# Kernel optimization log

Measured on AMD Instinct MI355X. Metric: run time of the kernel, lower is better.

Reference implementation:

```python
import jax, jax.numpy as jnp
import numpy as np

V, E, H, B, T, C = 50000, 100, 128, 128, 1024, 2


def setup_inputs() -> dict:
    key = jax.random.key(0)
    ks = jax.random.split(key, 32)
    rn = lambda k, shape: jax.random.normal(k, shape, jnp.float32) * 0.05
    inp = {}
    inp["x"] = jax.random.randint(ks[0], (B, T), 0, V)
    inp["emb"] = rn(ks[1], (V, E))
    i = 2
    for l, d_in in enumerate([E, 2 * H]):
        for sfx in ["", "_rev"]:
            inp[f"w_ih_l{l}{sfx}"] = rn(ks[i], (4 * H, d_in)); i += 1
            inp[f"w_hh_l{l}{sfx}"] = rn(ks[i], (4 * H, H)); i += 1
            inp[f"b_ih_l{l}{sfx}"] = rn(ks[i], (4 * H,)); i += 1
            inp[f"b_hh_l{l}{sfx}"] = rn(ks[i], (4 * H,)); i += 1
    inp["fc_w"] = rn(ks[i], (C, 2 * H))
    inp["fc_b"] = rn(ks[i + 1], (C,))
    return inp


def _lstm_dir(x, w_ih, w_hh, b_ih, b_hh, reverse):
    # x: [B, T, D]; PyTorch gate order: i, f, g, o
    Bn = x.shape[0]
    Hn = w_hh.shape[1]
    xp = jnp.einsum('btd,gd->btg', x, w_ih) + b_ih + b_hh  # [B, T, 4H], input proj hoisted out of scan
    xp = jnp.swapaxes(xp, 0, 1)  # [T, B, 4H]

    def step(carry, xt):
        h, c = carry
        g = xt + h @ w_hh.T
        i, f, gg, o = jnp.split(g, 4, axis=-1)
        c = jax.nn.sigmoid(f) * c + jax.nn.sigmoid(i) * jnp.tanh(gg)
        h = jax.nn.sigmoid(o) * jnp.tanh(c)
        return (h, c), h

    init = (jnp.zeros((Bn, Hn), x.dtype), jnp.zeros((Bn, Hn), x.dtype))
    (hT, cT), hs = jax.lax.scan(step, init, xp, reverse=reverse)
    return jnp.swapaxes(hs, 0, 1), hT  # [B, T, H], final hidden [B, H]


def reference(x, emb,
              w_ih_l0, w_hh_l0, b_ih_l0, b_hh_l0,
              w_ih_l0_rev, w_hh_l0_rev, b_ih_l0_rev, b_hh_l0_rev,
              w_ih_l1, w_hh_l1, b_ih_l1, b_hh_l1,
              w_ih_l1_rev, w_hh_l1_rev, b_ih_l1_rev, b_hh_l1_rev,
              fc_w, fc_b):
    h = emb[x]  # [B, T, E]
    # layer 0 (dropout between layers is identity in eval mode)
    f0, _ = _lstm_dir(h, w_ih_l0, w_hh_l0, b_ih_l0, b_hh_l0, False)
    b0, _ = _lstm_dir(h, w_ih_l0_rev, w_hh_l0_rev, b_ih_l0_rev, b_hh_l0_rev, True)
    h = jnp.concatenate([f0, b0], axis=-1)  # [B, T, 2H]
    # layer 1; final hidden states match torch hidden[-2] (fwd) and hidden[-1] (bwd)
    _, hf = _lstm_dir(h, w_ih_l1, w_hh_l1, b_ih_l1, b_hh_l1, False)
    _, hb = _lstm_dir(h, w_ih_l1_rev, w_hh_l1_rev, b_ih_l1_rev, b_hh_l1_rev, True)
    combined = jnp.concatenate([hf, hb], axis=-1)  # [B, 2H]
    return combined @ fc_w.T + fc_b  # [B, C]
```

## Files before the change

kernel.cpp:

```cpp
#include <hip/hip_runtime.h>
#include <hip/hip_bf16.h>
#include <stdint.h>


typedef unsigned short u16;
typedef short bf16x8 __attribute__((ext_vector_type(8)));
typedef unsigned short ushort8v __attribute__((ext_vector_type(8)));
typedef float f32x4 __attribute__((ext_vector_type(4)));
typedef float f32x2 __attribute__((ext_vector_type(2)));

#define NB 128
#define NT 1024
#define NH 128
#define TC 128
#define NCHUNK (NT / TC)
#define SMEM_BYTES 54656

#define L2E  1.44269504088896f
#define L2E2 2.88539008177793f

__device__ __forceinline__ u16 f2bf(float f) {
  union { float f; unsigned int i; } v; v.f = f;
  unsigned int i = v.i;
  return (u16)((i + 0x7FFFu + ((i >> 16) & 1u)) >> 16);
}

#if __has_builtin(__builtin_amdgcn_exp2f)
__device__ __forceinline__ float fast_exp2(float x) { return __builtin_amdgcn_exp2f(x); }
#else
__device__ __forceinline__ float fast_exp2(float x) { return exp2f(x); }
#endif
#if __has_builtin(__builtin_amdgcn_rcpf)
__device__ __forceinline__ float fast_rcp(float x) { return __builtin_amdgcn_rcpf(x); }
#else
__device__ __forceinline__ float fast_rcp(float x) { return 1.0f / x; }
#endif

__device__ __forceinline__ void sync_lds() {
  __builtin_amdgcn_s_waitcnt(0xc07f);
  __builtin_amdgcn_s_barrier();
}

__global__ void padw_kernel(const float* __restrict__ w0, const float* __restrict__ w1,
                            u16* __restrict__ out) {
  int idx = blockIdx.x * 256 + threadIdx.x;
  int d = idx >> 16;
  int n = (idx >> 7) & 511;
  int k = idx & 127;
  float sc = ((n >> 7) == 2) ? L2E2 : L2E;
  const float* w = d ? w1 : w0;
  out[idx] = (k < 100) ? f2bf(w[n * 100 + k] * sc) : (u16)0;
}

__global__ void cvt6_kernel(const float* s0, const float* s1, const float* s2,
                            const float* s3, const float* s4, const float* s5,
                            u16* d0, u16* d1, u16* d2, u16* d3, u16* d4, u16* d5,
                            int n0, int n1, int n2, int n3, int n4, int n5) {
  int y = blockIdx.y;
  const float* s; u16* d; int n; int gs;
  switch (y) {
    case 0: s = s0; d = d0; n = n0; gs = 14; break;
    case 1: s = s1; d = d1; n = n1; gs = 14; break;
    case 2: s = s2; d = d2; n = n2; gs = 14; break;
    case 3: s = s3; d = d3; n = n3; gs = 14; break;
    case 4: s = s4; d = d4; n = n4; gs = 15; break;
    default: s = s5; d = d5; n = n5; gs = 15; break;
  }
  int i = blockIdx.x * 256 + threadIdx.x;
  if (i < n) {
    float sc = (((i >> gs) & 3) == 2) ? L2E2 : L2E;
    d[i] = f2bf(s[i] * sc);
  }
}

template <int PK, int LL>
__global__ __launch_bounds__(512, 2) void fused_chunk(
    int do_lstm, int lc, int pc,
    const float* __restrict__ Aemb, const u16* __restrict__ Ah,
    const int* __restrict__ X,
    const u16* __restrict__ W0, const u16* __restrict__ W1,
    const float* __restrict__ bih0, const float* __restrict__ bhh0,
    const float* __restrict__ bih1, const float* __restrict__ bhh1,
    u16* __restrict__ xpc0, u16* __restrict__ xpc1,
    const u16* __restrict__ WHH0, const u16* __restrict__ WHH1,
    u16* __restrict__ OUT, float* __restrict__ FINALS,
    u16* __restrict__ HS, float* __restrict__ CS)
{
  extern __shared__ __align__(16) unsigned char smem[];

  const int tid = threadIdx.x;
  const int lane = tid & 63, wv = tid >> 6;
  const int l15 = lane & 15, q = lane >> 4;

  if (blockIdx.x >= 32) {
    constexpr int BK = 64;
    constexpr int LDA = 72;
    constexpr bool GATHER = (PK == 128);
    u16* As = (u16*)smem;
    u16* Bs = As + 128 * LDA;
    int* toks = (int*)(Bs + 128 * LDA);

    const int pb = blockIdx.x - 32;
    const int b = pb & 127;
    const int gate = (pb >> 7) & 3;
    const int nt0 = gate * 128;
    const int dir = pb >> 9;
    const u16* W = dir ? W1 : W0;
    u16* XPC = (pc & 1) ? xpc1 : xpc0;

    const int wr = wv >> 2, wc = wv & 3;

    if (GATHER) {
      if (tid < 128) {
        int t = dir ? (NT - 1 - pc * TC - tid) : (pc * TC + tid);
        toks[tid] = X[b * NT + t];
      }
    }

    f32x4 acc[4][2];
#pragma unroll
    for (int a = 0; a < 4; a++)
#pragma unroll
      for (int bb = 0; bb < 2; bb++)
        acc[a][bb] = (f32x4){0.f, 0.f, 0.f, 0.f};

    const int srow = tid >> 3;
    const int sseg = (tid & 7) * 8;

    for (int k0 = 0; k0 < PK; k0 += BK) {
      __syncthreads();
#pragma unroll
      for (int p = 0; p < 2; p++) {
        int row = srow + p * 64;
        if (GATHER) {
          int tok = toks[row];
          const float* er = Aemb + (size_t)tok * 100;
          int kb = k0 + sseg;
          union { ushort8v v; u16 e[8]; } tu;
          if (kb + 8 <= 100) {
            f32x4 a0 = *(const f32x4*)&er[kb];
            f32x4 a1 = *(const f32x4*)&er[kb + 4];
#pragma unroll
            for (int j = 0; j < 4; j++) { tu.e[j] = f2bf(a0[j]); tu.e[4 + j] = f2bf(a1[j]); }
          } else {
#pragma unroll
            for (int j = 0; j < 8; j++) tu.e[j] = (kb + j < 100) ? f2bf(er[kb + j]) : (u16)0;
          }
          *(ushort8v*)&As[row * LDA + sseg] = tu.v;
        } else {
          int t = dir ? (NT - 1 - pc * TC - row) : (pc * TC + row);
          const u16* srcA = Ah + (size_t)(b * NT + t) * PK + k0 + sseg;
          *(ushort8v*)&As[row * LDA + sseg] = *(const ushort8v*)srcA;
        }
        const u16* srcB = W + (size_t)(nt0 + row) * PK + k0 + sseg;
        *(ushort8v*)&Bs[row * LDA + sseg] = *(const ushort8v*)srcB;
      }
      __syncthreads();
#pragma unroll
      for (int kk = 0; kk < BK; kk += 32) {
        bf16x8 af[4], bfr[2];
#pragma unroll
        for (int mt = 0; mt < 4; mt++)
          af[mt] = *(const bf16x8*)&As[(wr * 64 + mt * 16 + l15) * LDA + kk + q * 8];
#pragma unroll
        for (int nt = 0; nt < 2; nt++)
          bfr[nt] = *(const bf16x8*)&Bs[(wc * 32 + nt * 16 + l15) * LDA + kk + q * 8];
#pragma unroll
        for (int mt = 0; mt < 4; mt++)
#pragma unroll
          for (int nt = 0; nt < 2; nt++)
            acc[mt][nt] = __builtin_amdgcn_mfma_f32_16x16x32_bf16(af[mt], bfr[nt], acc[mt][nt], 0, 0, 0);
      }
    }

    const float* bih = dir ? bih1 : bih0;
    const float* bhh = dir ? bhh1 : bhh0;
    const float gsc = (gate == 2) ? L2E2 : L2E;
    const int rb = b & 7;
    u16* xo = XPC + (size_t)(dir * 16 + (b >> 3)) * TC * 4096
                  + ((rb >> 1) & 1) * 64 + ((rb >> 2) & 1) * 32 + (rb & 1) + l15 * 2;
#pragma unroll
    for (int nt = 0; nt < 2; nt++) {
      int col = wc * 32 + nt * 16 + l15;
      int n = nt0 + col;
      float bias = (bih[n] + bhh[n]) * gsc;
      int bnt = ((wc * 2 + nt) * 4 + gate) * 128;
#pragma unroll
      for (int mt = 0; mt < 4; mt++) {
        int slb = wr * 64 + mt * 16 + q * 4;
#pragma unroll
        for (int r = 0; r < 4; r++)
          xo[(size_t)(slb + r) * 4096 + bnt] = f2bf(acc[mt][nt][r] + bias);
      }
    }
    return;
  }

  if (!do_lstm) return;

  __builtin_amdgcn_s_setprio(3);

  const int wg = blockIdx.x & 15, dir = blockIdx.x >> 4;
  const int hc = 16 * wv + l15;
  const u16* XPC = (lc & 1) ? xpc1 : xpc0;

  const int row0 = ((lane >> 4) & 1) * 4 + (lane >> 5) * 2;

  const u16* Wp = dir ? WHH1 : WHH0;
  bf16x8 wf[4][4];
#pragma unroll
  for (int gi = 0; gi < 4; gi++)
#pragma unroll
    for (int kt = 0; kt < 4; kt++)
      wf[gi][kt] = *(const bf16x8*)&Wp[(gi * 128 + hc) * 128 + kt * 32 + q * 8];

  u16* hb = (u16*)smem;

  const int g0 = (dir * 128 + wg * 8 + row0) * 128 + hc;
  f32x2 cst2;
  if (lc == 0) {
    for (int i = tid; i < 2 * 8 * 136; i += 512) hb[i] = 0;
    cst2 = (f32x2){0.f, 0.f};
  } else {
    hb[row0 * 136 + hc] = HS[g0];
    hb[(row0 + 1) * 136 + hc] = HS[g0 + 128];
    cst2[0] = CS[g0];
    cst2[1] = CS[g0 + 128];
  }

  const u16* xb = XPC + (size_t)(dir * 16 + wg) * TC * 4096 + wv * 512 + lane * 2;

#define LDXP(dst, s) do {                                        \
    const u16* nb_ = xb + (size_t)(s) * 4096;                    \
    _Pragma("unroll")                                            \
    for (int gi_ = 0; gi_ < 4; gi_++)                            \
      (dst)[gi_] = *(const unsigned int*)(nb_ + gi_ * 128);      \
  } while (0)

  unsigned int xp[4][4];
  LDXP(xp[0], 0);
  LDXP(xp[1], 1);
  LDXP(xp[2], 2);

  const int t0 = dir ? (NT - 1 - lc * TC) : (lc * TC);
  const int tstep = dir ? -256 : 256;
  u16* optr[2];
  if (LL == 0) {
#pragma unroll
    for (int rr = 0; rr < 2; rr++)
      optr[rr] = OUT + ((size_t)(wg * 8 + row0 + rr) * NT + t0) * 256 + dir * 128 + hc;
  }

  const f32x4 zero4 = {0.f, 0.f, 0.f, 0.f};
  const bool hi32 = (lane >= 32);
  const int arow = (l15 & 7) * 136;

  __syncthreads();

  int p = 0;
#pragma unroll 1
  for (int sl = 0; sl < TC; sl += 4) {
#pragma unroll
    for (int jj = 0; jj < 4; jj++) {
      const int scur = sl + jj;

      const unsigned int* xcur = xp[jj];
      f32x2 xv[4];
#pragma unroll
      for (int gi = 0; gi < 4; gi++) {
        union { unsigned int u; float f; } lo, hi;
        lo.u = xcur[gi] << 16;
        hi.u = xcur[gi] & 0xFFFF0000u;
        xv[gi][0] = lo.f; xv[gi][1] = hi.f;
      }
      {
        int sn = scur + 3; if (sn > TC - 1) sn = TC - 1;
        LDXP(xp[(jj + 3) & 3], sn);
      }

      bf16x8 ah[4];
#pragma unroll
      for (int kt = 0; kt < 4; kt++)
        ah[kt] = *(const bf16x8*)&hb[p * 1088 + arow + kt * 32 + q * 8];

      f32x4 acc[4];
#pragma unroll
      for (int gi = 0; gi < 4; gi++) {
        acc[gi] = __builtin_amdgcn_mfma_f32_16x16x32_bf16(ah[0], wf[gi][0], zero4, 0, 0, 0);
#pragma unroll
        for (int kt = 1; kt < 4; kt++)
          acc[gi] = __builtin_amdgcn_mfma_f32_16x16x32_bf16(ah[kt], wf[gi][kt], acc[gi], 0, 0, 0);
      }

      f32x2 ar[4];
#pragma unroll
      for (int gi = 0; gi < 4; gi++) {
        ar[gi][0] = hi32 ? acc[gi][2] : acc[gi][0];
        ar[gi][1] = hi32 ? acc[gi][3] : acc[gi][1];
      }

      f32x2 pi = ar[0] + xv[0];
      f32x2 pf = ar[1] + xv[1];
      f32x2 pg = ar[2] + xv[2];
      f32x2 po = ar[3] + xv[3];
      f32x2 ei, ef, eg, eo;
      ei[0] = fast_exp2(pi[0]); ei[1] = fast_exp2(pi[1]);
      ef[0] = fast_exp2(pf[0]); ef[1] = fast_exp2(pf[1]);
      eg[0] = fast_exp2(pg[0]); eg[1] = fast_exp2(pg[1]);
      eo[0] = fast_exp2(po[0]); eo[1] = fast_exp2(po[1]);
      f32x2 A  = 1.f + ef;
      f32x2 Bv = 1.f + ei;
      f32x2 Cg = 1.f + eg;
      f32x2 BC = Bv * Cg;
      f32x2 num = cst2 * ef * BC + ei * (eg - 1.f) * A;
      f32x2 den = A * BC;
      f32x2 rden; rden[0] = fast_rcp(den[0]); rden[1] = fast_rcp(den[1]);
      f32x2 cn = num * rden;
      cst2 = cn;
      f32x2 tc2 = L2E2 * cn;
      f32x2 ec; ec[0] = fast_exp2(tc2[0]); ec[1] = fast_exp2(tc2[1]);
      f32x2 d2 = (1.f + eo) * (1.f + ec);
      f32x2 r2; r2[0] = fast_rcp(d2[0]); r2[1] = fast_rcp(d2[1]);
      f32x2 hv2 = eo * (ec - 1.f) * r2;

      u16 hbv0 = f2bf(hv2[0]);
      u16 hbv1 = f2bf(hv2[1]);
      u16* hn = hb + (p ^ 1) * 1088;
      hn[row0 * 136 + hc] = hbv0;
      hn[(row0 + 1) * 136 + hc] = hbv1;
      if (LL == 0) {
        *optr[0] = hbv0; optr[0] += tstep;
        *optr[1] = hbv1; optr[1] += tstep;
      }
      if (scur == TC - 1) {
        HS[g0] = hbv0;
        HS[g0 + 128] = hbv1;
        CS[g0] = cst2[0];
        CS[g0 + 128] = cst2[1];
        if (LL == 1 && lc == NCHUNK - 1) {
          FINALS[(wg * 8 + row0) * 256 + dir * 128 + hc] = hv2[0];
          FINALS[(wg * 8 + row0 + 1) * 256 + dir * 128 + hc] = hv2[1];
        }
      }
      sync_lds();
      p ^= 1;
    }
  }
#undef LDXP
}

__global__ void fc_kernel(const float* __restrict__ finals, const float* __restrict__ fcw,
                          const float* __restrict__ fcb, float* __restrict__ out) {
  int tid = threadIdx.x;
  int b = tid >> 1, cc = tid & 1;
  float s = fcb[cc];
  for (int k = 0; k < 256; k++) s += finals[b * 256 + k] * fcw[cc * 256 + k];
  out[b * 2 + cc] = s;
}

extern "C" void kernel_launch(void* const* d_in, const int* in_sizes, int n_in,
                              void* d_out, int out_size, void* d_ws, size_t ws_size,
                              hipStream_t stream) {
  const int*   x        = (const int*)d_in[0];
  const float* emb      = (const float*)d_in[1];
  const float* w_ih_l0  = (const float*)d_in[2];
  const float* w_hh_l0  = (const float*)d_in[3];
  const float* b_ih_l0  = (const float*)d_in[4];
  const float* b_hh_l0  = (const float*)d_in[5];
  const float* w_ih_l0r = (const float*)d_in[6];
  const float* w_hh_l0r = (const float*)d_in[7];
  const float* b_ih_l0r = (const float*)d_in[8];
  const float* b_hh_l0r = (const float*)d_in[9];
  const float* w_ih_l1  = (const float*)d_in[10];
  const float* w_hh_l1  = (const float*)d_in[11];
  const float* b_ih_l1  = (const float*)d_in[12];
  const float* b_hh_l1  = (const float*)d_in[13];
  const float* w_ih_l1r = (const float*)d_in[14];
  const float* w_hh_l1r = (const float*)d_in[15];
  const float* b_ih_l1r = (const float*)d_in[16];
  const float* b_hh_l1r = (const float*)d_in[17];
  const float* fc_w     = (const float*)d_in[18];
  const float* fc_b     = (const float*)d_in[19];
  float* out = (float*)d_out;

  char* ws = (char*)d_ws;
  size_t off = 0;
  u16*   h1cat = (u16*)(ws + off);   off += 67108864;
  u16*   xpc0  = (u16*)(ws + off);   off += 33554432;
  u16*   xpc1  = (u16*)(ws + off);   off += 33554432;
  u16*   w0pad = (u16*)(ws + off);   off += 262144;
  u16*   wih1b = (u16*)(ws + off);   off += 524288;
  u16*   whhb  = (u16*)(ws + off);   off += 524288;
  u16*   hs    = (u16*)(ws + off);   off += 65536;
  float* cs    = (float*)(ws + off); off += 131072;
  float* fin   = (float*)(ws + off); off += 131072;
  if (ws_size < off) return;

  hipLaunchKernelGGL(padw_kernel, dim3(512), dim3(256), 0, stream,
                     w_ih_l0, w_ih_l0r, w0pad);
  hipLaunchKernelGGL(cvt6_kernel, dim3(512, 6), dim3(256), 0, stream,
                     w_hh_l0, w_hh_l0r, w_hh_l1, w_hh_l1r, w_ih_l1, w_ih_l1r,
                     whhb, whhb + 65536, whhb + 131072, whhb + 196608,
                     wih1b, wih1b + 131072,
                     65536, 65536, 65536, 65536, 131072, 131072);

  for (int k = 0; k <= NCHUNK; k++) {
    int do_proj = (k < NCHUNK);
    int do_lstm = (k > 0);
    hipLaunchKernelGGL((fused_chunk<128, 0>), dim3(do_proj ? 1056 : 32), dim3(512),
                       SMEM_BYTES, stream,
                       do_lstm, k - 1, k,
                       emb, (const u16*)nullptr, x, w0pad, w0pad + 65536,
                       b_ih_l0, b_hh_l0, b_ih_l0r, b_hh_l0r,
                       xpc0, xpc1, whhb, whhb + 65536,
                       h1cat, fin, hs, cs);
  }
  for (int k = 0; k <= NCHUNK; k++) {
    int do_proj = (k < NCHUNK);
    int do_lstm = (k > 0);
    hipLaunchKernelGGL((fused_chunk<256, 1>), dim3(do_proj ? 1056 : 32), dim3(512),
                       SMEM_BYTES, stream,
                       do_lstm, k - 1, k,
                       (const float*)nullptr, h1cat, (const int*)nullptr,
                       wih1b, wih1b + 131072,
                       b_ih_l1, b_hh_l1, b_ih_l1r, b_hh_l1r,
                       xpc0, xpc1, whhb + 131072, whhb + 196608,
                       h1cat, fin, hs, cs);
  }
  hipLaunchKernelGGL(fc_kernel, dim3(1), dim3(256), 0, stream, fin, fc_w, fc_b, out);
}
```

Baseline: 1.418 ms.

## Run both LSTM directions in one block per batch group, interleaved

The recurrent part now uses 16 workgroups instead of 32. Each workgroup processes both the forward and reverse directions for its 8 batch rows, holding both W_hh sets in registers and interleaving the two independent recurrences within each timestep. The intent is to fill the latency of the serial MFMA-then-activation dependency chain with independent work from the other direction, and to share one LDS barrier across both. In exchange it doubles register use for weights and per-step work per block, reduces the prefetch depth of the xp buffer from 3 steps to 2, and halves the number of CUs doing the recurrence.

```diff
diff --git a/kernel.cpp b/kernel.cpp
--- a/kernel.cpp
+++ b/kernel.cpp
@@ -92,7 +92,7 @@
   const int lane = tid & 63, wv = tid >> 6;
   const int l15 = lane & 15, q = lane >> 4;
 
-  if (blockIdx.x >= 32) {
+  if (blockIdx.x >= 16) {
     constexpr int BK = 64;
     constexpr int LDA = 72;
     constexpr bool GATHER = (PK == 128);
@@ -100,7 +100,7 @@
     u16* Bs = As + 128 * LDA;
     int* toks = (int*)(Bs + 128 * LDA);
 
-    const int pb = blockIdx.x - 32;
+    const int pb = blockIdx.x - 16;
     const int b = pb & 127;
     const int gate = (pb >> 7) & 3;
     const int nt0 = gate * 128;
@@ -200,55 +200,72 @@
 
   __builtin_amdgcn_s_setprio(3);
 
-  const int wg = blockIdx.x & 15, dir = blockIdx.x >> 4;
+  const int wg = blockIdx.x;
   const int hc = 16 * wv + l15;
   const u16* XPC = (lc & 1) ? xpc1 : xpc0;
 
   const int row0 = ((lane >> 4) & 1) * 4 + (lane >> 5) * 2;
 
-  const u16* Wp = dir ? WHH1 : WHH0;
-  bf16x8 wf[4][4];
-#pragma unroll
-  for (int gi = 0; gi < 4; gi++)
-#pragma unroll
-    for (int kt = 0; kt < 4; kt++)
-      wf[gi][kt] = *(const bf16x8*)&Wp[(gi * 128 + hc) * 128 + kt * 32 + q * 8];
+  bf16x8 wf[2][4][4];
+#pragma unroll
+  for (int d = 0; d < 2; d++) {
+    const u16* Wp = d ? WHH1 : WHH0;
+#pragma unroll
+    for (int gi = 0; gi < 4; gi++)
+#pragma unroll
+      for (int kt = 0; kt < 4; kt++)
+        wf[d][gi][kt] = *(const bf16x8*)&Wp[(gi * 128 + hc) * 128 + kt * 32 + q * 8];
+  }
 
   u16* hb = (u16*)smem;
 
-  const int g0 = (dir * 128 + wg * 8 + row0) * 128 + hc;
-  f32x2 cst2;
+  int g0[2];
+  f32x2 cst[2];
   if (lc == 0) {
-    for (int i = tid; i < 2 * 8 * 136; i += 512) hb[i] = 0;
-    cst2 = (f32x2){0.f, 0.f};
+    for (int i = tid; i < 2 * 2 * 1088; i += 512) hb[i] = 0;
+#pragma unroll
+    for (int d = 0; d < 2; d++) {
+      g0[d] = (d * 128 + wg * 8 + row0) * 128 + hc;
+      cst[d] = (f32x2){0.f, 0.f};
+    }
   } else {
-    hb[row0 * 136 + hc] = HS[g0];
-    hb[(row0 + 1) * 136 + hc] = HS[g0 + 128];
-    cst2[0] = CS[g0];
-    cst2[1] = CS[g0 + 128];
-  }
-
-  const u16* xb = XPC + (size_t)(dir * 16 + wg) * TC * 4096 + wv * 512 + lane * 2;
-
-#define LDXP(dst, s) do {                                        \
-    const u16* nb_ = xb + (size_t)(s) * 4096;                    \
-    _Pragma("unroll")                                            \
-    for (int gi_ = 0; gi_ < 4; gi_++)                            \
-      (dst)[gi_] = *(const unsigned int*)(nb_ + gi_ * 128);      \
+#pragma unroll
+    for (int d = 0; d < 2; d++) {
+      g0[d] = (d * 128 + wg * 8 + row0) * 128 + hc;
+      hb[d * 2176 + row0 * 136 + hc] = HS[g0[d]];
+      hb[d * 2176 + (row0 + 1) * 136 + hc] = HS[g0[d] + 128];
+      cst[d][0] = CS[g0[d]];
+      cst[d][1] = CS[g0[d] + 128];
+    }
+  }
+
+  const u16* xb[2];
+  xb[0] = XPC + (size_t)(wg) * TC * 4096 + wv * 512 + lane * 2;
+  xb[1] = XPC + (size_t)(16 + wg) * TC * 4096 + wv * 512 + lane * 2;
+
+#define LDXP(dst, s) do {                                            \
+    _Pragma("unroll")                                                \
+    for (int d_ = 0; d_ < 2; d_++) {                                 \
+      const u16* nb_ = xb[d_] + (size_t)(s) * 4096;                  \
+      _Pragma("unroll")                                              \
+      for (int gi_ = 0; gi_ < 4; gi_++)                              \
+        (dst)[d_][gi_] = *(const unsigned int*)(nb_ + gi_ * 128);    \
+    }                                                                \
   } while (0)
 
-  unsigned int xp[4][4];
+  unsigned int xp[2][2][4];
   LDXP(xp[0], 0);
   LDXP(xp[1], 1);
-  LDXP(xp[2], 2);
-
-  const int t0 = dir ? (NT - 1 - lc * TC) : (lc * TC);
-  const int tstep = dir ? -256 : 256;
-  u16* optr[2];
+
+  u16* optr[2][2];
   if (LL == 0) {
 #pragma unroll
-    for (int rr = 0; rr < 2; rr++)
-      optr[rr] = OUT + ((size_t)(wg * 8 + row0 + rr) * NT + t0) * 256 + dir * 128 + hc;
+    for (int d = 0; d < 2; d++) {
+      const int t0d = d ? (NT - 1 - lc * TC) : (lc * TC);
+#pragma unroll
+      for (int rr = 0; rr < 2; rr++)
+        optr[d][rr] = OUT + ((size_t)(wg * 8 + row0 + rr) * NT + t0d) * 256 + d * 128 + hc;
+    }
   }
 
   const f32x4 zero4 = {0.f, 0.f, 0.f, 0.f};
@@ -259,87 +276,97 @@
 
   int p = 0;
 #pragma unroll 1
-  for (int sl = 0; sl < TC; sl += 4) {
-#pragma unroll
-    for (int jj = 0; jj < 4; jj++) {
+  for (int sl = 0; sl < TC; sl += 2) {
+#pragma unroll
+    for (int jj = 0; jj < 2; jj++) {
       const int scur = sl + jj;
 
-      const unsigned int* xcur = xp[jj];
-      f32x2 xv[4];
-#pragma unroll
-      for (int gi = 0; gi < 4; gi++) {
-        union { unsigned int u; float f; } lo, hi;
-        lo.u = xcur[gi] << 16;
-        hi.u = xcur[gi] & 0xFFFF0000u;
-        xv[gi][0] = lo.f; xv[gi][1] = hi.f;
-      }
+      f32x2 xv[2][4];
+#pragma unroll
+      for (int d = 0; d < 2; d++)
+#pragma unroll
+        for (int gi = 0; gi < 4; gi++) {
+          union { unsigned int u; float f; } lo, hi;
+          lo.u = xp[jj][d][gi] << 16;
+          hi.u = xp[jj][d][gi] & 0xFFFF0000u;
+          xv[d][gi][0] = lo.f; xv[d][gi][1] = hi.f;
+        }
       {
-        int sn = scur + 3; if (sn > TC - 1) sn = TC - 1;
-        LDXP(xp[(jj + 3) & 3], sn);
-      }
-
-      bf16x8 ah[4];
-#pragma unroll
-      for (int kt = 0; kt < 4; kt++)
-        ah[kt] = *(const bf16x8*)&hb[p * 1088 + arow + kt * 32 + q * 8];
-
-      f32x4 acc[4];
-#pragma unroll
-      for (int gi = 0; gi < 4; gi++) {
-        acc[gi] = __builtin_amdgcn_mfma_f32_16x16x32_bf16(ah[0], wf[gi][0], zero4, 0, 0, 0);
-#pragma unroll
-        for (int kt = 1; kt < 4; kt++)
-          acc[gi] = __builtin_amdgcn_mfma_f32_16x16x32_bf16(ah[kt], wf[gi][kt], acc[gi], 0, 0, 0);
-      }
-
-      f32x2 ar[4];
-#pragma unroll
-      for (int gi = 0; gi < 4; gi++) {
-        ar[gi][0] = hi32 ? acc[gi][2] : acc[gi][0];
-        ar[gi][1] = hi32 ? acc[gi][3] : acc[gi][1];
-      }
-
-      f32x2 pi = ar[0] + xv[0];
-      f32x2 pf = ar[1] + xv[1];
-      f32x2 pg = ar[2] + xv[2];
-      f32x2 po = ar[3] + xv[3];
-      f32x2 ei, ef, eg, eo;
-      ei[0] = fast_exp2(pi[0]); ei[1] = fast_exp2(pi[1]);
-      ef[0] = fast_exp2(pf[0]); ef[1] = fast_exp2(pf[1]);
-      eg[0] = fast_exp2(pg[0]); eg[1] = fast_exp2(pg[1]);
-      eo[0] = fast_exp2(po[0]); eo[1] = fast_exp2(po[1]);
-      f32x2 A  = 1.f + ef;
-      f32x2 Bv = 1.f + ei;
-      f32x2 Cg = 1.f + eg;
-      f32x2 BC = Bv * Cg;
-      f32x2 num = cst2 * ef * BC + ei * (eg - 1.f) * A;
-      f32x2 den = A * BC;
-      f32x2 rden; rden[0] = fast_rcp(den[0]); rden[1] = fast_rcp(den[1]);
-      f32x2 cn = num * rden;
-      cst2 = cn;
-      f32x2 tc2 = L2E2 * cn;
-      f32x2 ec; ec[0] = fast_exp2(tc2[0]); ec[1] = fast_exp2(tc2[1]);
-      f32x2 d2 = (1.f + eo) * (1.f + ec);
-      f32x2 r2; r2[0] = fast_rcp(d2[0]); r2[1] = fast_rcp(d2[1]);
-      f32x2 hv2 = eo * (ec - 1.f) * r2;
-
-      u16 hbv0 = f2bf(hv2[0]);
-      u16 hbv1 = f2bf(hv2[1]);
-      u16* hn = hb + (p ^ 1) * 1088;
-      hn[row0 * 136 + hc] = hbv0;
-      hn[(row0 + 1) * 136 + hc] = hbv1;
-      if (LL == 0) {
-        *optr[0] = hbv0; optr[0] += tstep;
-        *optr[1] = hbv1; optr[1] += tstep;
-      }
-      if (scur == TC - 1) {
-        HS[g0] = hbv0;
-        HS[g0 + 128] = hbv1;
-        CS[g0] = cst2[0];
-        CS[g0 + 128] = cst2[1];
-        if (LL == 1 && lc == NCHUNK - 1) {
-          FINALS[(wg * 8 + row0) * 256 + dir * 128 + hc] = hv2[0];
-          FINALS[(wg * 8 + row0 + 1) * 256 + dir * 128 + hc] = hv2[1];
+        int sn = scur + 2; if (sn > TC - 1) sn = TC - 1;
+        LDXP(xp[jj], sn);
+      }
+
+      f32x2 hv2s[2];
+#pragma unroll
+      for (int d = 0; d < 2; d++) {
+        bf16x8 ah[4];
+#pragma unroll
+        for (int kt = 0; kt < 4; kt++)
+          ah[kt] = *(const bf16x8*)&hb[d * 2176 + p * 1088 + arow + kt * 32 + q * 8];
+
+        f32x4 acc[4];
+#pragma unroll
+        for (int gi = 0; gi < 4; gi++) {
+          acc[gi] = __builtin_amdgcn_mfma_f32_16x16x32_bf16(ah[0], wf[d][gi][0], zero4, 0, 0, 0);
+#pragma unroll
+          for (int kt = 1; kt < 4; kt++)
+            acc[gi] = __builtin_amdgcn_mfma_f32_16x16x32_bf16(ah[kt], wf[d][gi][kt], acc[gi], 0, 0, 0);
+        }
+
+        f32x2 ar[4];
+#pragma unroll
+        for (int gi = 0; gi < 4; gi++) {
+          ar[gi][0] = hi32 ? acc[gi][2] : acc[gi][0];
+          ar[gi][1] = hi32 ? acc[gi][3] : acc[gi][1];
+        }
+
+        f32x2 pi = ar[0] + xv[d][0];
+        f32x2 pf = ar[1] + xv[d][1];
+        f32x2 pg = ar[2] + xv[d][2];
+        f32x2 po = ar[3] + xv[d][3];
+        f32x2 ei, ef, eg, eo;
+        ei[0] = fast_exp2(pi[0]); ei[1] = fast_exp2(pi[1]);
+        ef[0] = fast_exp2(pf[0]); ef[1] = fast_exp2(pf[1]);
+        eg[0] = fast_exp2(pg[0]); eg[1] = fast_exp2(pg[1]);
+        eo[0] = fast_exp2(po[0]); eo[1] = fast_exp2(po[1]);
+        f32x2 A  = 1.f + ef;
+        f32x2 Bv = 1.f + ei;
+        f32x2 Cg = 1.f + eg;
+        f32x2 BC = Bv * Cg;
+        f32x2 num = cst[d] * ef * BC + ei * (eg - 1.f) * A;
+        f32x2 den = A * BC;
+        f32x2 rden; rden[0] = fast_rcp(den[0]); rden[1] = fast_rcp(den[1]);
+        f32x2 cn = num * rden;
+        cst[d] = cn;
+        f32x2 tc2 = L2E2 * cn;
+        f32x2 ec; ec[0] = fast_exp2(tc2[0]); ec[1] = fast_exp2(tc2[1]);
+        f32x2 d2 = (1.f + eo) * (1.f + ec);
+        f32x2 r2; r2[0] = fast_rcp(d2[0]); r2[1] = fast_rcp(d2[1]);
+        hv2s[d] = eo * (ec - 1.f) * r2;
+      }
+
+#pragma unroll
+      for (int d = 0; d < 2; d++) {
+        u16 hbv0 = f2bf(hv2s[d][0]);
+        u16 hbv1 = f2bf(hv2s[d][1]);
+        u16* hn = hb + d * 2176 + (p ^ 1) * 1088;
+        hn[row0 * 136 + hc] = hbv0;
+        hn[(row0 + 1) * 136 + hc] = hbv1;
+        if (LL == 0) {
+          *optr[d][0] = hbv0;
+          *optr[d][1] = hbv1;
+          optr[d][0] += (d ? -256 : 256);
+          optr[d][1] += (d ? -256 : 256);
+        }
+        if (scur == TC - 1) {
+          HS[g0[d]] = hbv0;
+          HS[g0[d] + 128] = hbv1;
+          CS[g0[d]] = cst[d][0];
+          CS[g0[d] + 128] = cst[d][1];
+          if (LL == 1 && lc == NCHUNK - 1) {
+            FINALS[(wg * 8 + row0) * 256 + d * 128 + hc] = hv2s[d][0];
+            FINALS[(wg * 8 + row0 + 1) * 256 + d * 128 + hc] = hv2s[d][1];
+          }
         }
       }
       sync_lds();
@@ -407,7 +434,7 @@
   for (int k = 0; k <= NCHUNK; k++) {
     int do_proj = (k < NCHUNK);
     int do_lstm = (k > 0);
-    hipLaunchKernelGGL((fused_chunk<128, 0>), dim3(do_proj ? 1056 : 32), dim3(512),
+    hipLaunchKernelGGL((fused_chunk<128, 0>), dim3(do_proj ? 1040 : 16), dim3(512),
                        SMEM_BYTES, stream,
                        do_lstm, k - 1, k,
                        emb, (const u16*)nullptr, x, w0pad, w0pad + 65536,
@@ -418,7 +445,7 @@
   for (int k = 0; k <= NCHUNK; k++) {
     int do_proj = (k < NCHUNK);
     int do_lstm = (k > 0);
-    hipLaunchKernelGGL((fused_chunk<256, 1>), dim3(do_proj ? 1056 : 32), dim3(512),
+    hipLaunchKernelGGL((fused_chunk<256, 1>), dim3(do_proj ? 1040 : 16), dim3(512),
                        SMEM_BYTES, stream,
                        do_lstm, k - 1, k,
                        (const float*)nullptr, h1cat, (const int*)nullptr,
```

Result: slower. 2.610 ms (+84.0%).
